# Kernel optimization log

Measured on AMD Instinct MI355X. Metric: run time of the kernel, lower is better.

Reference implementation:

```python
import jax, jax.numpy as jnp
import numpy as np
from jax import lax

B, S, D = 4, 128, 256
POOL = 3


def conv_block(x, w, b, stride, pool_k):
    # x: (N, Cin, H, W), w: (Cout, Cin, kh, kw)
    y = lax.conv_general_dilated(
        x, w, window_strides=(stride, stride), padding='VALID',
        dimension_numbers=('NCHW', 'OIHW', 'NCHW'))
    y = y + b[None, :, None, None]
    y = jax.nn.gelu(y, approximate=False)  # torch GELU default is exact
    # MaxPool2d(kernel_size=pool_k) -> stride = pool_k, VALID
    y = lax.reduce_window(y, -jnp.inf, lax.max,
                          (1, 1, pool_k, pool_k), (1, 1, pool_k, pool_k), 'VALID')
    return y


def setup_inputs() -> dict:
    key = jax.random.key(0)
    ks = jax.random.split(key, 8)
    token_features = jax.random.normal(ks[0], (B, S, D), dtype=jnp.float32)
    type_embedds = jax.random.normal(ks[1], (B, S, D), dtype=jnp.float32)
    # Conv2dFeatures(depth=3, num_channels=16, start_kernel=3, start_stride=2, pool_kernel=3)
    w1 = jax.random.normal(ks[2], (16, 1, 3, 3), dtype=jnp.float32) * 0.1
    b1 = jax.random.normal(ks[3], (16,), dtype=jnp.float32) * 0.01
    w2 = jax.random.normal(ks[4], (32, 16, 3, 3), dtype=jnp.float32) * 0.05
    b2 = jax.random.normal(ks[5], (32,), dtype=jnp.float32) * 0.01
    w3 = jax.random.normal(ks[6], (32, 32, 3, 3), dtype=jnp.float32) * 0.05
    b3 = jax.random.normal(ks[7], (32,), dtype=jnp.float32) * 0.01
    return dict(token_features=token_features, type_embedds=type_embedds,
                w1=w1, b1=b1, w2=w2, b2=b2, w3=w3, b3=b3)


def reference(token_features, type_embedds, w1, b1, w2, b2, w3, b3):
    b, s, d = type_embedds.shape
    # Outter2dFusion: fused[n,s,i,j] = type_embedds[n,s,i] * token_features[n,s,j]
    fused = jnp.einsum('bsi,bsj->bsij', type_embedds, token_features)
    # Conv stack applied per seq position with in_channels=1 == one batched conv
    x = fused.reshape(b * s, 1, d, d)
    x = conv_block(x, w1, b1, stride=2, pool_k=POOL)
    x = conv_block(x, w2, b2, stride=1, pool_k=POOL)
    x = conv_block(x, w3, b3, stride=1, pool_k=POOL)
    # Dropout is identity in eval mode
    return x.reshape(b, s, -1)
```

## Files before the change

kernel.cpp:

```cpp
#include <hip/hip_runtime.h>
#include <math.h>


#define NIMG 512

__device__ __forceinline__ float gelu_exact(float x) {
    return 0.5f * x * (1.0f + erff(x * 0.70710678118654752f));
}
__device__ __forceinline__ float pool_gelu(float vmin, float vmax) {
    return fmaxf(gelu_exact(vmin), gelu_exact(vmax));
}

__global__ __launch_bounds__(256) void k1_fused(const float* __restrict__ tok,
                                                const float* __restrict__ typ,
                                                const float* __restrict__ w1,
                                                const float* __restrict__ b1,
                                                float* __restrict__ s1) {
    const int blk = blockIdx.x;
    const int img = blk >> 1;
    const int py0 = (blk & 1) * 21;
    const int tid = threadIdx.x;
    const int c     = tid >> 4;
    const int pslot = tid & 15;

    float wv[9];
#pragma unroll
    for (int k = 0; k < 9; ++k) wv[k] = w1[c * 9 + k];
    const float bias = b1[c];

    const float* frow = tok + img * 256;
    const float* trow = typ + img * 256;

    float g[3][3][3];
    int pxv[3];
#pragma unroll
    for (int s = 0; s < 3; ++s) {
        const int px = pslot + 16 * s;
        pxv[s] = px;
        const int pe = px < 42 ? px : 41;
        float f7[7];
#pragma unroll
        for (int q = 0; q < 7; ++q) f7[q] = frow[6 * pe + q];
#pragma unroll
        for (int di = 0; di < 3; ++di)
#pragma unroll
            for (int wx = 0; wx < 3; ++wx)
                g[s][di][wx] = wv[di * 3 + 0] * f7[2 * wx]
                             + wv[di * 3 + 1] * f7[2 * wx + 1]
                             + wv[di * 3 + 2] * f7[2 * wx + 2];
    }

    float* orow = s1 + ((size_t)img * 16 + c) * (42 * 44);
    for (int py = py0; py < py0 + 21; ++py) {
        float ts[7];
#pragma unroll
        for (int q = 0; q < 7; ++q) ts[q] = trow[6 * py + q];
#pragma unroll
        for (int s = 0; s < 3; ++s) {
            float vmin = INFINITY, vmax = -INFINITY;
#pragma unroll
            for (int wy = 0; wy < 3; ++wy) {
#pragma unroll
                for (int wx = 0; wx < 3; ++wx) {
                    float v = ts[2 * wy] * g[s][0][wx];
                    v = fmaf(ts[2 * wy + 1], g[s][1][wx], v);
                    v = fmaf(ts[2 * wy + 2], g[s][2][wx], v);
                    vmin = fminf(vmin, v);
                    vmax = fmaxf(vmax, v);
                }
            }
            if (pxv[s] < 42)
                orow[py * 44 + pxv[s]] = pool_gelu(vmin + bias, vmax + bias);
        }
    }
}

__global__ __launch_bounds__(256) void k2_conv(const float* __restrict__ s1,
                                               const float* __restrict__ w2,
                                               const float* __restrict__ b2,
                                               float* __restrict__ s2) {
    const int blk = blockIdx.x;
    const int img = blk >> 1;
    const int cog = blk & 1;
    __shared__ float4 slab4[462];
    float* slab = (float*)slab4;

    const int tid  = threadIdx.x;
    const int lane = tid & 63;
    const int grp  = tid >> 6;

    int base[3], valid[3], py[3], px[3];
#pragma unroll
    for (int tI = 0; tI < 3; ++tI) {
        const int cc0 = lane + 64 * tI;
        valid[tI] = (cc0 < 169);
        const int cc = valid[tI] ? cc0 : 168;
        py[tI] = cc % 13;
        px[tI] = cc / 13;
        base[tI] = py[tI] * 132 + px[tI] * 3;
    }

    float acc[4][3][9];
#pragma unroll
    for (int a = 0; a < 4; ++a)
#pragma unroll
        for (int tI = 0; tI < 3; ++tI)
#pragma unroll
            for (int k = 0; k < 9; ++k) acc[a][tI][k] = 0.f;

    const float* s1img = s1 + (size_t)img * 16 * 1848;

    for (int cin = 0; cin < 16; ++cin) {
        __syncthreads();
        const float4* src = (const float4*)(s1img + cin * 1848);
        for (int i = tid; i < 462; i += 256) slab4[i] = src[i];
        __syncthreads();

        const int wbase = __builtin_amdgcn_readfirstlane((cog * 16 + grp) * 144 + cin * 9);
        float wv[4][9];
#pragma unroll
        for (int a = 0; a < 4; ++a)
#pragma unroll
            for (int k = 0; k < 9; ++k) wv[a][k] = w2[wbase + a * 576 + k];

#pragma unroll
        for (int tI = 0; tI < 3; ++tI) {
            float win[5][5];
#pragma unroll
            for (int r = 0; r < 5; ++r)
#pragma unroll
                for (int c2 = 0; c2 < 5; ++c2)
                    win[r][c2] = slab[base[tI] + r * 44 + c2];
#pragma unroll
            for (int wy = 0; wy < 3; ++wy)
#pragma unroll
                for (int wx = 0; wx < 3; ++wx)
#pragma unroll
                    for (int dy = 0; dy < 3; ++dy)
#pragma unroll
                        for (int dx = 0; dx < 3; ++dx) {
                            const float v = win[wy + dy][wx + dx];
#pragma unroll
                            for (int a = 0; a < 4; ++a)
                                acc[a][tI][wy * 3 + wx] =
                                    fmaf(v, wv[a][dy * 3 + dx], acc[a][tI][wy * 3 + wx]);
                        }
        }
    }

#pragma unroll
    for (int tI = 0; tI < 3; ++tI) {
        if (valid[tI]) {
#pragma unroll
            for (int a = 0; a < 4; ++a) {
                float vmin = INFINITY, vmax = -INFINITY;
#pragma unroll
                for (int k = 0; k < 9; ++k) {
                    vmin = fminf(vmin, acc[a][tI][k]);
                    vmax = fmaxf(vmax, acc[a][tI][k]);
                }
                const int co = cog * 16 + grp + 4 * a;
                const float b = b2[co];
                s2[((img * 32 + co) * 13 + py[tI]) * 13 + px[tI]] =
                    pool_gelu(vmin + b, vmax + b);
            }
        }
    }
}

__global__ __launch_bounds__(192) void k3_conv(const float* __restrict__ s2,
                                               const float* __restrict__ w3,
                                               const float* __restrict__ b3,
                                               float* __restrict__ out) {
    const int img = blockIdx.x;
    __shared__ float4 s2l4[1352];
    __shared__ float wl[32 * 32 * 9];
    float* s2l = (float*)s2l4;

    const int tid = threadIdx.x;
    const float4* src = (const float4*)(s2 + (size_t)img * 5408);
    for (int i = tid; i < 1352; i += 192) s2l4[i] = src[i];
    for (int i = tid; i < 9216; i += 192) wl[i] = w3[i];
    __syncthreads();

    if (tid < 144) {
        const int cp   = tid / 9;
        const int cell = tid % 9;
        const int cy = cell / 3, cx = cell % 3;
        const int base = (3 * cy) * 13 + 3 * cx;
        const int co0 = 2 * cp, co1 = 2 * cp + 1;

        float acc[2][9];
#pragma unroll
        for (int a = 0; a < 2; ++a)
#pragma unroll
            for (int k = 0; k < 9; ++k) acc[a][k] = 0.f;

        for (int cin = 0; cin < 32; ++cin) {
            float win[5][5];
#pragma unroll
            for (int r = 0; r < 5; ++r)
#pragma unroll
                for (int c2 = 0; c2 < 5; ++c2)
                    win[r][c2] = s2l[cin * 169 + base + r * 13 + c2];
            float wk[2][9];
#pragma unroll
            for (int k = 0; k < 9; ++k) {
                wk[0][k] = wl[(co0 * 32 + cin) * 9 + k];
                wk[1][k] = wl[(co1 * 32 + cin) * 9 + k];
            }
#pragma unroll
            for (int wy = 0; wy < 3; ++wy)
#pragma unroll
                for (int wx = 0; wx < 3; ++wx)
#pragma unroll
                    for (int dy = 0; dy < 3; ++dy)
#pragma unroll
                        for (int dx = 0; dx < 3; ++dx) {
                            const float v = win[wy + dy][wx + dx];
                            acc[0][wy * 3 + wx] = fmaf(v, wk[0][dy * 3 + dx], acc[0][wy * 3 + wx]);
                            acc[1][wy * 3 + wx] = fmaf(v, wk[1][dy * 3 + dx], acc[1][wy * 3 + wx]);
                        }
        }

#pragma unroll
        for (int a = 0; a < 2; ++a) {
            float vmin = INFINITY, vmax = -INFINITY;
#pragma unroll
            for (int k = 0; k < 9; ++k) {
                vmin = fminf(vmin, acc[a][k]);
                vmax = fmaxf(vmax, acc[a][k]);
            }
            const int co = a ? co1 : co0;
            const float b = b3[co];
            out[(size_t)img * 288 + co * 9 + cell] = pool_gelu(vmin + b, vmax + b);
        }
    }
}

extern "C" void kernel_launch(void* const* d_in, const int* in_sizes, int n_in,
                              void* d_out, int out_size, void* d_ws, size_t ws_size,
                              hipStream_t stream) {
    const float* tok = (const float*)d_in[0];
    const float* typ = (const float*)d_in[1];
    const float* w1  = (const float*)d_in[2];
    const float* b1  = (const float*)d_in[3];
    const float* w2  = (const float*)d_in[4];
    const float* b2  = (const float*)d_in[5];
    const float* w3  = (const float*)d_in[6];
    const float* b3  = (const float*)d_in[7];
    float* out = (float*)d_out;

    float* s1 = (float*)d_ws;
    float* s2 = s1 + (size_t)NIMG * 16 * 42 * 44;

    k1_fused<<<dim3(NIMG * 2), dim3(256), 0, stream>>>(tok, typ, w1, b1, s1);
    k2_conv<<<dim3(NIMG * 2), dim3(256), 0, stream>>>(s1, w2, b2, s2);
    k3_conv<<<dim3(NIMG), dim3(192), 0, stream>>>(s2, w3, b3, out);
}
```

Before: 259.8 us.

## Double-buffer conv2 input slabs with async global-to-LDS loads

The second conv kernel now prefetches the next input channel's slab straight into a second LDS buffer with global_load_lds while computing on the current one. This replaces the synchronous copy-then-barrier per channel and is meant to overlap global memory latency with the FMA work. The output-pixel mapping is also swapped so consecutive lanes step along x, which makes the s2 stores contiguous and changes the LDS read pattern. The async loads fetch 512 float4 per channel where 462 are needed, so the last channel of the last image can read past the end of s1. LDS use also doubles.

```diff
diff --git a/kernel.cpp b/kernel.cpp
--- a/kernel.cpp
+++ b/kernel.cpp
@@ -9,6 +9,12 @@
 }
 __device__ __forceinline__ float pool_gelu(float vmin, float vmax) {
     return fmaxf(gelu_exact(vmin), gelu_exact(vmax));
+}
+
+typedef __attribute__((address_space(3))) char lds_char;
+typedef const __attribute__((address_space(1))) char glb_char;
+__device__ __forceinline__ void gl_lds16(const void* g, void* l) {
+    __builtin_amdgcn_global_load_lds((glb_char*)g, (lds_char*)l, 16, 0, 0);
 }
 
 __global__ __launch_bounds__(256) void k1_fused(const float* __restrict__ tok,
@@ -82,12 +88,12 @@
     const int blk = blockIdx.x;
     const int img = blk >> 1;
     const int cog = blk & 1;
-    __shared__ float4 slab4[462];
-    float* slab = (float*)slab4;
+    __shared__ float4 slab4[2][512];
 
     const int tid  = threadIdx.x;
     const int lane = tid & 63;
     const int grp  = tid >> 6;
+    const int wbase64 = tid & ~63;
 
     int base[3], valid[3], py[3], px[3];
 #pragma unroll
@@ -95,8 +101,8 @@
         const int cc0 = lane + 64 * tI;
         valid[tI] = (cc0 < 169);
         const int cc = valid[tI] ? cc0 : 168;
-        py[tI] = cc % 13;
-        px[tI] = cc / 13;
+        py[tI] = cc / 13;
+        px[tI] = cc % 13;
         base[tI] = py[tI] * 132 + px[tI] * 3;
     }
 
@@ -110,19 +116,31 @@
 
     const float* s1img = s1 + (size_t)img * 16 * 1848;
 
+    {
+        const char* src = (const char*)(s1img);
+        gl_lds16(src + (size_t)tid * 16,        (char*)&slab4[0][0] + (size_t)wbase64 * 16);
+        gl_lds16(src + (size_t)(256 + tid) * 16,(char*)&slab4[0][256] + (size_t)wbase64 * 16);
+    }
+    asm volatile("s_waitcnt vmcnt(0)" ::: "memory");
+    __syncthreads();
+
+#pragma unroll 1
     for (int cin = 0; cin < 16; ++cin) {
-        __syncthreads();
-        const float4* src = (const float4*)(s1img + cin * 1848);
-        for (int i = tid; i < 462; i += 256) slab4[i] = src[i];
-        __syncthreads();
-
-        const int wbase = __builtin_amdgcn_readfirstlane((cog * 16 + grp) * 144 + cin * 9);
+        const int cur = cin & 1;
+        if (cin < 15) {
+            const char* src = (const char*)(s1img + (cin + 1) * 1848);
+            gl_lds16(src + (size_t)tid * 16,         (char*)&slab4[cur ^ 1][0] + (size_t)wbase64 * 16);
+            gl_lds16(src + (size_t)(256 + tid) * 16, (char*)&slab4[cur ^ 1][256] + (size_t)wbase64 * 16);
+        }
+
+        const int wb = __builtin_amdgcn_readfirstlane((cog * 16 + grp) * 144 + cin * 9);
         float wv[4][9];
 #pragma unroll
         for (int a = 0; a < 4; ++a)
 #pragma unroll
-            for (int k = 0; k < 9; ++k) wv[a][k] = w2[wbase + a * 576 + k];
-
+            for (int k = 0; k < 9; ++k) wv[a][k] = w2[wb + a * 576 + k];
+
+        const float* slab = (const float*)&slab4[cur][0];
 #pragma unroll
         for (int tI = 0; tI < 3; ++tI) {
             float win[5][5];
@@ -146,6 +164,9 @@
                                     fmaf(v, wv[a][dy * 3 + dx], acc[a][tI][wy * 3 + wx]);
                         }
         }
+
+        asm volatile("s_waitcnt vmcnt(0)" ::: "memory");
+        __syncthreads();
     }
 
 #pragma unroll
```

After: 254.4 us. 2.1% less time.
